# Kernel tuning notes

Hardware: AMD Instinct MI355X
Metric: run time of the kernel (lower is better)

## Reference

```python
import jax, jax.numpy as jnp
import numpy as np

N_USERS = 100000
N_ITEMS = 50000
N_NODES = N_USERS + N_ITEMS
EMB_DIM = 64
N_EDGES = 4000000
N_LAYERS = 3
BATCH = 4096


def setup_inputs() -> dict:
    key = jax.random.key(0)
    k = jax.random.split(key, 7)
    return {
        "user_emb": jax.random.normal(k[0], (N_USERS, EMB_DIM), dtype=jnp.float32) * 0.1,
        "item_emb": jax.random.normal(k[1], (N_ITEMS, EMB_DIM), dtype=jnp.float32) * 0.1,
        "vals": jax.random.uniform(k[2], (N_EDGES,), dtype=jnp.float32),
        "src": jax.random.randint(k[3], (N_EDGES,), 0, N_NODES, dtype=jnp.int32),
        "dst": jax.random.randint(k[4], (N_EDGES,), 0, N_NODES, dtype=jnp.int32),
        "users": jax.random.randint(k[5], (BATCH,), 0, N_USERS, dtype=jnp.int32),
        "items": jax.random.randint(k[6], (BATCH,), 0, N_ITEMS, dtype=jnp.int32),
    }


def _propagate(user_emb, item_emb, vals, src, dst):
    # all_emb: [N, D]; sparse adjacency A given as COO (src -> dst, weight vals)
    all_emb = jnp.concatenate([user_emb, item_emb], axis=0)
    acc = all_emb  # running sum over layers (layer 0 included)
    emb = all_emb
    for _ in range(N_LAYERS):
        # SpMM: out[d] = sum_{e: dst[e]==d} vals[e] * emb[src[e]]
        msgs = vals[:, None] * emb[src]               # [E, D]
        emb = jax.ops.segment_sum(msgs, dst, num_segments=N_NODES)
        acc = acc + emb
    light_out = acc / jnp.float32(N_LAYERS + 1)       # mean over stacked layers
    return light_out[:N_USERS], light_out[N_USERS:]


def reference(user_emb, item_emb, vals, src, dst, users, items):
    all_users, all_items = _propagate(user_emb, item_emb, vals, src, dst)
    u = all_users[users]                              # [B, D]
    i = all_items[items]                              # [B, D]
    gamma = jnp.sum(u * i, axis=1)                    # [B]
    return gamma
```

## Files before the change

### kernel.cpp

```cpp
#include <hip/hip_runtime.h>
#include <hip/hip_bf16.h>

#define N_USERS 100000
#define N_ITEMS 50000
#define N_NODES 150000
#define DIM 64
#define N_EDGES 4000000
#define BATCH 4096

#define NBKT 256
#define BW 588
#define STRIDE 16640
#define PA_EDGES 4096
#define PA_ITER 16
#define PA_BLOCKS ((N_EDGES + PA_EDGES - 1) / PA_EDGES)
#define CVT_THREADS (N_NODES * DIM / 8)
#define CVT_BLOCKS 512
#define BS_ITER 32
#define SPMM_BLOCKS ((N_NODES * 64 + 255) / 256)
#define MARK_BLOCKS ((2 * BATCH * 64) / 256)
#define BMAP_WORDS ((N_NODES + 31) / 32)

__device__ __forceinline__ float blo(unsigned int u) { return __uint_as_float(u << 16); }
__device__ __forceinline__ float bhi(unsigned int u) { return __uint_as_float(u & 0xffff0000u); }
__device__ __forceinline__ unsigned int f2b(float f) {
    unsigned int x = __float_as_uint(f);
    return (x + 0x7fffu + ((x >> 16) & 1u)) >> 16;
}
__device__ __forceinline__ unsigned int pack2(float a, float b) {
    return f2b(a) | (f2b(b) << 16);
}

typedef float v2f __attribute__((ext_vector_type(2)));

__global__ void __launch_bounds__(256, 4) k_partition(
        const int* __restrict__ src, const int* __restrict__ dst,
        const float* __restrict__ vals,
        int* __restrict__ gcur, int2* __restrict__ tmp) {
    __shared__ int cnt[NBKT];
    __shared__ int base_s[NBKT];
    __shared__ int off_s[NBKT];
    __shared__ int2 rec_s[PA_EDGES];
    __shared__ unsigned char bin_s[PA_EDGES];
    int t = threadIdx.x;
    int myb[PA_ITER];
    int mykey[PA_ITER];
    int myval[PA_ITER];
    size_t base = (size_t)blockIdx.x * PA_EDGES;
#pragma unroll
    for (int it = 0; it < PA_ITER; it++) {
        size_t i = base + (size_t)it * 256 + t;
        if (i < N_EDGES) {
            myb[it] = __builtin_nontemporal_load(dst + i);
            mykey[it] = __builtin_nontemporal_load(src + i);
            myval[it] = __float_as_int(__builtin_nontemporal_load(vals + i));
        } else {
            myb[it] = -1;
        }
    }
    for (int i = t; i < NBKT; i += 256) cnt[i] = 0;
    __syncthreads();
#pragma unroll
    for (int it = 0; it < PA_ITER; it++) {
        int d = myb[it];
        if (d >= 0) {
            int b = d / BW;
            mykey[it] = (mykey[it] << 10) | (d - b * BW);
            myb[it] = b;
            atomicAdd(&cnt[b], 1);
        }
    }
    __syncthreads();
    {
        int bb = (t + blockIdx.x * 37) & (NBKT - 1);
        int c = cnt[bb];
        base_s[bb] = (c > 0) ? atomicAdd(&gcur[bb], c) : 0;
    }
    if (t < 64) {
        int lane = t;
        int carry = 0;
        for (int c = 0; c < NBKT / 64; c++) {
            int i = c * 64 + lane;
            int x = cnt[i];
            int incl = x;
            for (int o = 1; o < 64; o <<= 1) {
                int y = __shfl_up(incl, o);
                if (lane >= o) incl += y;
            }
            off_s[i] = carry + incl - x;
            carry += __shfl(incl, 63);
        }
    }
    __syncthreads();
    for (int i = t; i < NBKT; i += 256) cnt[i] = 0;
    __syncthreads();
#pragma unroll
    for (int it = 0; it < PA_ITER; it++) {
        int b = myb[it];
        if (b >= 0) {
            int pos = off_s[b] + atomicAdd(&cnt[b], 1);
            rec_s[pos] = make_int2(mykey[it], myval[it]);
            bin_s[pos] = (unsigned char)b;
        }
    }
    __syncthreads();
    int nrec = off_s[NBKT - 1] + cnt[NBKT - 1];
    for (int i = t; i < nrec; i += 256) {
        int2 r = rec_s[i];
        int b = bin_s[i];
        tmp[(size_t)b * STRIDE + base_s[b] + (i - off_s[b])] = r;
    }
}

__global__ void k_bsortcvt(const int2* __restrict__ tmp, const int* __restrict__ gcur,
                           int* __restrict__ row_ptr, int2* __restrict__ fin,
                           const float* __restrict__ uemb, const float* __restrict__ iemb,
                           ushort* __restrict__ ebf0) {
    __shared__ int cnt[BW + 64];
    __shared__ int off[BW + 64];
    __shared__ int gbase_s;
    extern __shared__ int2 rec2[];
    int b = blockIdx.x, t = threadIdx.x;
    if (b >= NBKT) {
        for (int idx = (b - NBKT) * 512 + t; idx < CVT_THREADS; idx += CVT_BLOCKS * 512) {
            int i = idx * 8;
            const float* srcp = (i < N_USERS * DIM) ? (uemb + i) : (iemb + (i - N_USERS * DIM));
            float4 v0, v1;
            v0.x = __builtin_nontemporal_load(srcp + 0);
            v0.y = __builtin_nontemporal_load(srcp + 1);
            v0.z = __builtin_nontemporal_load(srcp + 2);
            v0.w = __builtin_nontemporal_load(srcp + 3);
            v1.x = __builtin_nontemporal_load(srcp + 4);
            v1.y = __builtin_nontemporal_load(srcp + 5);
            v1.z = __builtin_nontemporal_load(srcp + 6);
            v1.w = __builtin_nontemporal_load(srcp + 7);
            uint4 p;
            p.x = pack2(v0.x, v0.y);
            p.y = pack2(v0.z, v0.w);
            p.z = pack2(v1.x, v1.y);
            p.w = pack2(v1.z, v1.w);
            *(uint4*)(ebf0 + i) = p;
        }
        return;
    }
    int node0 = b * BW;
    int nodes = min(BW, N_NODES - node0);
    int count = gcur[b];
    const int2* tb = tmp + (size_t)b * STRIDE;
    int2 myrec[BS_ITER];
#pragma unroll
    for (int it = 0; it < BS_ITER; it++) {
        int e = it * 512 + t;
        myrec[it] = (e < count) ? tb[e] : make_int2(-1, 0);
    }
    if (t < 64) {
        int ssum = 0;
#pragma unroll
        for (int j = 0; j < NBKT / 64; j++) {
            int idx = t * (NBKT / 64) + j;
            if (idx < b) ssum += gcur[idx];
        }
        for (int o = 32; o; o >>= 1) ssum += __shfl_xor(ssum, o);
        if (t == 0) gbase_s = ssum;
    }
    for (int i = t; i < BW + 64; i += 512) cnt[i] = 0;
    __syncthreads();
    int gbase = gbase_s;
#pragma unroll
    for (int it = 0; it < BS_ITER; it++)
        if (myrec[it].x >= 0) atomicAdd(&cnt[myrec[it].x & 1023], 1);
    for (int e = BS_ITER * 512 + t; e < count; e += 512)
        atomicAdd(&cnt[tb[e].x & 1023], 1);
    __syncthreads();
    if (t < 64) {
        int lane = t;
        int carry = 0;
        for (int c = 0; c < 10; c++) {
            int i = c * 64 + lane;
            int x = (i < nodes) ? cnt[i] : 0;
            int incl = x;
            for (int o = 1; o < 64; o <<= 1) {
                int y = __shfl_up(incl, o);
                if (lane >= o) incl += y;
            }
            if (i <= nodes) off[i] = carry + incl - x;
            carry += __shfl(incl, 63);
        }
    }
    __syncthreads();
    for (int i = t; i <= nodes; i += 512)
        if (node0 + i <= N_NODES) row_ptr[node0 + i] = gbase + off[i];
    __syncthreads();
#pragma unroll
    for (int it = 0; it < BS_ITER; it++) {
        int2 r = myrec[it];
        if (r.x >= 0) {
            int pos = atomicAdd(&off[r.x & 1023], 1);
            rec2[pos] = make_int2(r.x >> 10, r.y);
        }
    }
    for (int e = BS_ITER * 512 + t; e < count; e += 512) {
        int2 r = tb[e];
        int pos = atomicAdd(&off[r.x & 1023], 1);
        rec2[pos] = make_int2(r.x >> 10, r.y);
    }
    __syncthreads();
    for (int i = t; i < count; i += 512) fin[gbase + i] = rec2[i];
}


#define EDGE_FMA(r, u, A0, A1, A2, A3)                                        \
    {                                                                         \
        float vf = __int_as_float((r).y);                                     \
        v2f vv = {vf, vf};                                                    \
        v2f f0 = {blo((u).x), bhi((u).x)};                                    \
        v2f f1 = {blo((u).y), bhi((u).y)};                                    \
        v2f f2 = {blo((u).z), bhi((u).z)};                                    \
        v2f f3 = {blo((u).w), bhi((u).w)};                                    \
        A0 = __builtin_elementwise_fma(vv, f0, A0);                           \
        A1 = __builtin_elementwise_fma(vv, f1, A1);                           \
        A2 = __builtin_elementwise_fma(vv, f2, A2);                           \
        A3 = __builtin_elementwise_fma(vv, f3, A3);                           \
    }

#define GATHER16(basec, r) (*(const uint4*)((basec) + ((((unsigned int)(r).x) << 7) | qoff)))
#define REC8(basec, i) (*(const int2*)((basec) + (((unsigned int)(i)) << 3)))

#define BURST32(basec, e, end, last, X0, X1, X2, X3)                          \
    {                                                                         \
        int e1 = (e) + 8, e2 = (e) + 16, e3 = (e) + 24;                       \
        int2 ra = REC8(basec, (e));                                           \
        int2 rb = REC8(basec, min(e1, last));                                 \
        int2 rc = REC8(basec, min(e2, last));                                 \
        int2 rd = REC8(basec, min(e3, last));                                 \
        rb.y = (e1 < (end)) ? rb.y : 0;                                       \
        rc.y = (e2 < (end)) ? rc.y : 0;                                       \
        rd.y = (e3 < (end)) ? rd.y : 0;                                       \
        uint4 ua = GATHER16(einc, ra);                                        \
        uint4 ub = GATHER16(einc, rb);                                        \
        uint4 uc = GATHER16(einc, rc);                                        \
        uint4 ud = GATHER16(einc, rd);                                        \
        EDGE_FMA(ra, ua, X0, X1, X2, X3);                                     \
        EDGE_FMA(rb, ub, X0, X1, X2, X3);                                     \
        EDGE_FMA(rc, uc, X0, X1, X2, X3);                                     \
        EDGE_FMA(rd, ud, X0, X1, X2, X3);                                     \
        (e) += 32;                                                            \
    }

__global__ void k_spmm16(const ushort* __restrict__ ein, ushort* __restrict__ eout,
                         const int* __restrict__ row_ptr, const int2* __restrict__ fin,
                         const int* __restrict__ users, const int* __restrict__ items,
                         unsigned int* __restrict__ bmw, const unsigned int* __restrict__ bmr,
                         int mark_blocks) {
    if (blockIdx.x < (unsigned)mark_blocks) {
        int slot = (blockIdx.x * 256 + (int)threadIdx.x) >> 6;
        int lane = threadIdx.x & 63;
        if (slot < 2 * BATCH) {
            int node = (slot < BATCH) ? users[slot] : (items[slot - BATCH] + N_USERS);
            if (lane == 0) atomicOr(&bmw[node >> 5], 1u << (node & 31));
            int s0 = row_ptr[node], s1 = row_ptr[node + 1];
            for (int e = s0 + lane; e < s1; e += 64) {
                int s = fin[e].x;
                atomicOr(&bmw[s >> 5], 1u << (s & 31));
            }
        }
        return;
    }
    int wave = ((blockIdx.x - mark_blocks) * 256 + (int)threadIdx.x) >> 6;
    if (wave >= N_NODES) return;
    if (bmr && !((bmr[wave >> 5] >> (wave & 31)) & 1u)) return;
    int lane = threadIdx.x & 63;
    int g = lane >> 3;
    int q = lane & 7;
    unsigned int qoff = (unsigned int)q << 4;
    const char* einc = (const char*)ein;
    const char* finc = (const char*)fin;
    int start = row_ptr[wave], end = row_ptr[wave + 1];
    int last = max(start, end - 1);
    v2f A0 = {0.f, 0.f}, A1 = {0.f, 0.f}, A2 = {0.f, 0.f}, A3 = {0.f, 0.f};
    int e = start + g;
    while (e < end) BURST32(finc, e, end, last, A0, A1, A2, A3);
#pragma unroll
    for (int off = 8; off < 64; off <<= 1) {
        A0.x += __shfl_xor(A0.x, off);
        A0.y += __shfl_xor(A0.y, off);
        A1.x += __shfl_xor(A1.x, off);
        A1.y += __shfl_xor(A1.y, off);
        A2.x += __shfl_xor(A2.x, off);
        A2.y += __shfl_xor(A2.y, off);
        A3.x += __shfl_xor(A3.x, off);
        A3.y += __shfl_xor(A3.y, off);
    }
    if (lane < 8) {
        uint4 p;
        p.x = pack2(A0.x, A0.y);
        p.y = pack2(A1.x, A1.y);
        p.z = pack2(A2.x, A2.y);
        p.w = pack2(A3.x, A3.y);
        *(uint4*)(eout + (size_t)wave * DIM + q * 8) = p;
    }
}

__global__ void k_sampdot(const float* __restrict__ uemb, const float* __restrict__ iemb,
                          const ushort* __restrict__ ebf1, const ushort* __restrict__ ebf2,
                          const int* __restrict__ row_ptr, const int2* __restrict__ fin,
                          const int* __restrict__ users, const int* __restrict__ items,
                          float* __restrict__ out) {
    int b = (blockIdx.x * blockDim.x + threadIdx.x) >> 6;
    if (b >= BATCH) return;
    int lane = threadIdx.x & 63;
    int g = lane >> 3;
    int q = lane & 7;
    unsigned int qoff = (unsigned int)q << 4;
    const char* einc = (const char*)ebf2;
    const char* finc = (const char*)fin;
    int iu = users[b];
    int ii = items[b];
    int nu = iu, ni = ii + N_USERS;
    v2f A0 = {0.f, 0.f}, A1 = {0.f, 0.f}, A2 = {0.f, 0.f}, A3 = {0.f, 0.f};
    {
        int start = row_ptr[nu], end = row_ptr[nu + 1];
        int last = max(start, end - 1);
        int e = start + g;
        while (e < end) BURST32(finc, e, end, last, A0, A1, A2, A3);
    }
    v2f B0 = {0.f, 0.f}, B1 = {0.f, 0.f}, B2 = {0.f, 0.f}, B3 = {0.f, 0.f};
    {
        int start = row_ptr[ni], end = row_ptr[ni + 1];
        int last = max(start, end - 1);
        int e = start + g;
        while (e < end) BURST32(finc, e, end, last, B0, B1, B2, B3);
    }
#pragma unroll
    for (int off = 8; off < 64; off <<= 1) {
        A0.x += __shfl_xor(A0.x, off);
        A0.y += __shfl_xor(A0.y, off);
        A1.x += __shfl_xor(A1.x, off);
        A1.y += __shfl_xor(A1.y, off);
        A2.x += __shfl_xor(A2.x, off);
        A2.y += __shfl_xor(A2.y, off);
        A3.x += __shfl_xor(A3.x, off);
        A3.y += __shfl_xor(A3.y, off);
        B0.x += __shfl_xor(B0.x, off);
        B0.y += __shfl_xor(B0.y, off);
        B1.x += __shfl_xor(B1.x, off);
        B1.y += __shfl_xor(B1.y, off);
        B2.x += __shfl_xor(B2.x, off);
        B2.y += __shfl_xor(B2.y, off);
        B3.x += __shfl_xor(B3.x, off);
        B3.y += __shfl_xor(B3.y, off);
    }
    {
        const float4* fp = (const float4*)(uemb + (size_t)nu * DIM + q * 8);
        float4 fa = fp[0], fb = fp[1];
        uint4 u1 = *(const uint4*)(ebf1 + (size_t)nu * DIM + q * 8);
        uint4 u2 = *(const uint4*)(ebf2 + (size_t)nu * DIM + q * 8);
        A0.x += fa.x + blo(u1.x) + blo(u2.x); A0.y += fa.y + bhi(u1.x) + bhi(u2.x);
        A1.x += fa.z + blo(u1.y) + blo(u2.y); A1.y += fa.w + bhi(u1.y) + bhi(u2.y);
        A2.x += fb.x + blo(u1.z) + blo(u2.z); A2.y += fb.y + bhi(u1.z) + bhi(u2.z);
        A3.x += fb.z + blo(u1.w) + blo(u2.w); A3.y += fb.w + bhi(u1.w) + bhi(u2.w);
    }
    {
        const float4* fp = (const float4*)(iemb + (size_t)ii * DIM + q * 8);
        float4 fa = fp[0], fb = fp[1];
        uint4 u1 = *(const uint4*)(ebf1 + (size_t)ni * DIM + q * 8);
        uint4 u2 = *(const uint4*)(ebf2 + (size_t)ni * DIM + q * 8);
        B0.x += fa.x + blo(u1.x) + blo(u2.x); B0.y += fa.y + bhi(u1.x) + bhi(u2.x);
        B1.x += fa.z + blo(u1.y) + blo(u2.y); B1.y += fa.w + bhi(u1.y) + bhi(u2.y);
        B2.x += fb.x + blo(u1.z) + blo(u2.z); B2.y += fb.y + bhi(u1.z) + bhi(u2.z);
        B3.x += fb.z + blo(u1.w) + blo(u2.w); B3.y += fb.w + bhi(u1.w) + bhi(u2.w);
    }
    float p = A0.x * B0.x + A0.y * B0.y + A1.x * B1.x + A1.y * B1.y +
              A2.x * B2.x + A2.y * B2.y + A3.x * B3.x + A3.y * B3.y;
    p += __shfl_xor(p, 1);
    p += __shfl_xor(p, 2);
    p += __shfl_xor(p, 4);
    if (lane == 0) out[b] = p * (1.0f / 16.0f);
}


extern "C" void kernel_launch(void* const* d_in, const int* in_sizes, int n_in,
                              void* d_out, int out_size, void* d_ws, size_t ws_size,
                              hipStream_t stream) {
    const float* user_emb = (const float*)d_in[0];
    const float* item_emb = (const float*)d_in[1];
    const float* vals = (const float*)d_in[2];
    const int* src = (const int*)d_in[3];
    const int* dst = (const int*)d_in[4];
    const int* users = (const int*)d_in[5];
    const int* items = (const int*)d_in[6];
    float* out = (float*)d_out;

    char* ws = (char*)d_ws;
    size_t off = 0;
    auto alloc = [&](size_t bytes) {
        char* p = ws + off;
        off += (bytes + 255) & ~(size_t)255;
        return p;
    };
    ushort* ebf0 = (ushort*)alloc((size_t)N_NODES * DIM * 2);
    ushort* ebf1 = (ushort*)alloc((size_t)N_NODES * DIM * 2);
    ushort* ebf2 = (ushort*)alloc((size_t)N_NODES * DIM * 2);
    int2* fin = (int2*)alloc((size_t)N_EDGES * 8);
    int* row_ptr = (int*)alloc((size_t)(N_NODES + 1) * 4);
    int* gcur = (int*)alloc((size_t)NBKT * 4);
    unsigned int* bitmap = (unsigned int*)alloc((size_t)BMAP_WORDS * 4);
    int2* tmp = (int2*)ebf1;

    (void)hipMemsetAsync(gcur, 0, (size_t)NBKT * 4, stream);
    (void)hipMemsetAsync(bitmap, 0, (size_t)BMAP_WORDS * 4, stream);

    k_partition<<<PA_BLOCKS, 256, 0, stream>>>(src, dst, vals, gcur, tmp);
    k_bsortcvt<<<NBKT + CVT_BLOCKS, 512, (size_t)STRIDE * 8, stream>>>(
        tmp, gcur, row_ptr, fin, user_emb, item_emb, ebf0);

    k_spmm16<<<MARK_BLOCKS + SPMM_BLOCKS, 256, 0, stream>>>(
        ebf0, ebf1, row_ptr, fin, users, items, bitmap, nullptr, MARK_BLOCKS);
    k_spmm16<<<SPMM_BLOCKS, 256, 0, stream>>>(
        ebf1, ebf2, row_ptr, fin, users, items, nullptr, bitmap, 0);
    k_sampdot<<<(BATCH * 64 + 255) / 256, 256, 0, stream>>>(
        user_emb, item_emb, ebf1, ebf2, row_ptr, fin, users, items, out);
}
```

Baseline: 317.9 us.

## Move sample-neighbor bitmap marking into partition and bucket-sort kernels

Sampled user/item nodes are now flagged in a separate bitmap during the partition kernel. The bucket-sort kernel then marks the in-neighbors of those nodes using the locally sorted edge records held in shared memory. This removes the mark blocks that were prepended to the first SpMM launch, which re-read row_ptr and fin from global memory. The cost is an extra memset, another bitmap, and more atomics and synchronization work inside the bucket-sort kernel.

```diff
diff --git a/kernel.cpp b/kernel.cpp
--- a/kernel.cpp
+++ b/kernel.cpp
@@ -18,8 +18,8 @@
 #define CVT_BLOCKS 512
 #define BS_ITER 32
 #define SPMM_BLOCKS ((N_NODES * 64 + 255) / 256)
-#define MARK_BLOCKS ((2 * BATCH * 64) / 256)
 #define BMAP_WORDS ((N_NODES + 31) / 32)
+#define SLIST_CAP 256
 
 __device__ __forceinline__ float blo(unsigned int u) { return __uint_as_float(u << 16); }
 __device__ __forceinline__ float bhi(unsigned int u) { return __uint_as_float(u & 0xffff0000u); }
@@ -36,13 +36,22 @@
 __global__ void __launch_bounds__(256, 4) k_partition(
         const int* __restrict__ src, const int* __restrict__ dst,
         const float* __restrict__ vals,
-        int* __restrict__ gcur, int2* __restrict__ tmp) {
+        int* __restrict__ gcur, int2* __restrict__ tmp,
+        const int* __restrict__ users, const int* __restrict__ items,
+        unsigned int* __restrict__ sampbit) {
     __shared__ int cnt[NBKT];
     __shared__ int base_s[NBKT];
     __shared__ int off_s[NBKT];
     __shared__ int2 rec_s[PA_EDGES];
     __shared__ unsigned char bin_s[PA_EDGES];
     int t = threadIdx.x;
+    if (blockIdx.x < 32) {
+        int slot = blockIdx.x * 256 + t;
+        if (slot < 2 * BATCH) {
+            int node = (slot < BATCH) ? users[slot] : (items[slot - BATCH] + N_USERS);
+            atomicOr(&sampbit[node >> 5], 1u << (node & 31));
+        }
+    }
     int myb[PA_ITER];
     int mykey[PA_ITER];
     int myval[PA_ITER];
@@ -115,10 +124,14 @@
 __global__ void k_bsortcvt(const int2* __restrict__ tmp, const int* __restrict__ gcur,
                            int* __restrict__ row_ptr, int2* __restrict__ fin,
                            const float* __restrict__ uemb, const float* __restrict__ iemb,
-                           ushort* __restrict__ ebf0) {
+                           ushort* __restrict__ ebf0,
+                           const unsigned int* __restrict__ sampbit,
+                           unsigned int* __restrict__ bmw) {
     __shared__ int cnt[BW + 64];
     __shared__ int off[BW + 64];
     __shared__ int gbase_s;
+    __shared__ int sN[SLIST_CAP];
+    __shared__ int scnt_s;
     extern __shared__ int2 rec2[];
     int b = blockIdx.x, t = threadIdx.x;
     if (b >= NBKT) {
@@ -163,6 +176,7 @@
         for (int o = 32; o; o >>= 1) ssum += __shfl_xor(ssum, o);
         if (t == 0) gbase_s = ssum;
     }
+    if (t == 0) scnt_s = 0;
     for (int i = t; i < BW + 64; i += 512) cnt[i] = 0;
     __syncthreads();
     int gbase = gbase_s;
@@ -205,7 +219,34 @@
         rec2[pos] = make_int2(r.x >> 10, r.y);
     }
     __syncthreads();
+    for (int i = t; i < nodes; i += 512) {
+        int n = node0 + i;
+        if ((sampbit[n >> 5] >> (n & 31)) & 1u) {
+            atomicOr(&bmw[n >> 5], 1u << (n & 31));
+            int idx = atomicAdd(&scnt_s, 1);
+            if (idx < SLIST_CAP) {
+                sN[idx] = i;
+            } else {
+                int ls = (i == 0) ? 0 : off[i - 1], le = off[i];
+                for (int e = ls; e < le; e++) {
+                    int s = rec2[e].x;
+                    atomicOr(&bmw[s >> 5], 1u << (s & 31));
+                }
+            }
+        }
+    }
+    __syncthreads();
     for (int i = t; i < count; i += 512) fin[gbase + i] = rec2[i];
+    int sc = min(scnt_s, SLIST_CAP);
+    int wv = t >> 6, ln = t & 63;
+    for (int j = wv; j < sc; j += 8) {
+        int i = sN[j];
+        int ls = (i == 0) ? 0 : off[i - 1], le = off[i];
+        for (int e = ls + ln; e < le; e += 64) {
+            int s = rec2[e].x;
+            atomicOr(&bmw[s >> 5], 1u << (s & 31));
+        }
+    }
 }
 
 
@@ -249,24 +290,8 @@
 
 __global__ void k_spmm16(const ushort* __restrict__ ein, ushort* __restrict__ eout,
                          const int* __restrict__ row_ptr, const int2* __restrict__ fin,
-                         const int* __restrict__ users, const int* __restrict__ items,
-                         unsigned int* __restrict__ bmw, const unsigned int* __restrict__ bmr,
-                         int mark_blocks) {
-    if (blockIdx.x < (unsigned)mark_blocks) {
-        int slot = (blockIdx.x * 256 + (int)threadIdx.x) >> 6;
-        int lane = threadIdx.x & 63;
-        if (slot < 2 * BATCH) {
-            int node = (slot < BATCH) ? users[slot] : (items[slot - BATCH] + N_USERS);
-            if (lane == 0) atomicOr(&bmw[node >> 5], 1u << (node & 31));
-            int s0 = row_ptr[node], s1 = row_ptr[node + 1];
-            for (int e = s0 + lane; e < s1; e += 64) {
-                int s = fin[e].x;
-                atomicOr(&bmw[s >> 5], 1u << (s & 31));
-            }
-        }
-        return;
-    }
-    int wave = ((blockIdx.x - mark_blocks) * 256 + (int)threadIdx.x) >> 6;
+                         const unsigned int* __restrict__ bmr) {
+    int wave = (blockIdx.x * blockDim.x + threadIdx.x) >> 6;
     if (wave >= N_NODES) return;
     if (bmr && !((bmr[wave >> 5] >> (wave & 31)) & 1u)) return;
     int lane = threadIdx.x & 63;
@@ -404,20 +429,21 @@
     int2* fin = (int2*)alloc((size_t)N_EDGES * 8);
     int* row_ptr = (int*)alloc((size_t)(N_NODES + 1) * 4);
     int* gcur = (int*)alloc((size_t)NBKT * 4);
+    unsigned int* sampbit = (unsigned int*)alloc((size_t)BMAP_WORDS * 4);
     unsigned int* bitmap = (unsigned int*)alloc((size_t)BMAP_WORDS * 4);
     int2* tmp = (int2*)ebf1;
 
     (void)hipMemsetAsync(gcur, 0, (size_t)NBKT * 4, stream);
+    (void)hipMemsetAsync(sampbit, 0, (size_t)BMAP_WORDS * 4, stream);
     (void)hipMemsetAsync(bitmap, 0, (size_t)BMAP_WORDS * 4, stream);
 
-    k_partition<<<PA_BLOCKS, 256, 0, stream>>>(src, dst, vals, gcur, tmp);
+    k_partition<<<PA_BLOCKS, 256, 0, stream>>>(src, dst, vals, gcur, tmp,
+                                               users, items, sampbit);
     k_bsortcvt<<<NBKT + CVT_BLOCKS, 512, (size_t)STRIDE * 8, stream>>>(
-        tmp, gcur, row_ptr, fin, user_emb, item_emb, ebf0);
-
-    k_spmm16<<<MARK_BLOCKS + SPMM_BLOCKS, 256, 0, stream>>>(
-        ebf0, ebf1, row_ptr, fin, users, items, bitmap, nullptr, MARK_BLOCKS);
-    k_spmm16<<<SPMM_BLOCKS, 256, 0, stream>>>(
-        ebf1, ebf2, row_ptr, fin, users, items, nullptr, bitmap, 0);
+        tmp, gcur, row_ptr, fin, user_emb, item_emb, ebf0, sampbit, bitmap);
+
+    k_spmm16<<<SPMM_BLOCKS, 256, 0, stream>>>(ebf0, ebf1, row_ptr, fin, nullptr);
+    k_spmm16<<<SPMM_BLOCKS, 256, 0, stream>>>(ebf1, ebf2, row_ptr, fin, bitmap);
     k_sampdot<<<(BATCH * 64 + 255) / 256, 256, 0, stream>>>(
         user_emb, item_emb, ebf1, ebf2, row_ptr, fin, users, items, out);
 }
```

Measured after the change: 316.4 us. No clear change (-0.5%).
